# Optimization experiments

Measured on AMD Instinct MI355X. Metric: run time of the kernel, lower is better.

The kernel has to match this reference:

```python
import jax, jax.numpy as jnp
import numpy as np

D_MODEL = 1024
H = 16
D_K = D_MODEL // H
B, S = 1, 4096


def setup_inputs() -> dict:
    key = jax.random.key(0)
    ks = jax.random.split(key, 12)
    std = 1.0 / np.sqrt(D_MODEL)
    inp = {
        "q": jax.random.normal(ks[0], (B, S, D_MODEL), dtype=jnp.float32),
        "k": jax.random.normal(ks[1], (B, S, D_MODEL), dtype=jnp.float32),
        "v": jax.random.normal(ks[2], (B, S, D_MODEL), dtype=jnp.float32),
        "mask": jax.random.randint(ks[3], (B, 1, S, S), 0, 2).astype(bool),
        # nn.Linear params (torch convention: y = x @ W.T + b), weights [out, in]
        "wq": jax.random.uniform(ks[4], (D_MODEL, D_MODEL), jnp.float32, -std, std),
        "bq": jax.random.uniform(ks[5], (D_MODEL,), jnp.float32, -std, std),
        "wk": jax.random.uniform(ks[6], (D_MODEL, D_MODEL), jnp.float32, -std, std),
        "bk": jax.random.uniform(ks[7], (D_MODEL,), jnp.float32, -std, std),
        "wv": jax.random.uniform(ks[8], (D_MODEL, D_MODEL), jnp.float32, -std, std),
        "bv": jax.random.uniform(ks[9], (D_MODEL,), jnp.float32, -std, std),
        "wo": jax.random.uniform(ks[10], (D_MODEL, D_MODEL), jnp.float32, -std, std),
        "bo": jax.random.uniform(ks[11], (D_MODEL,), jnp.float32, -std, std),
    }
    return inp


def _split_heads(x):
    # [b, s, (h d)] -> [b, h, s, d]
    b, s, _ = x.shape
    return x.reshape(b, s, H, D_K).transpose(0, 2, 1, 3)


def reference(q, k, v, mask, wq, bq, wk, bk, wv, bv, wo, bo):
    b, s, d = q.shape
    qh = _split_heads(q @ wq.T + bq)
    kh = _split_heads(k @ wk.T + bk)
    vh = _split_heads(v @ wv.T + bv)
    # NOTE: original scales by sqrt(d_model), not sqrt(d_k) — keep faithful.
    score = jnp.einsum("bhqd,bhkd->bhqk", qh, kh) / jnp.sqrt(jnp.float32(d))
    score = jnp.where(mask, jnp.float32(-1e9), score)
    attn = jax.nn.softmax(score, axis=-1)  # dropout is identity in eval mode
    wv_out = jnp.einsum("bhqk,bhkd->bhqd", attn, vh)
    concat = wv_out.transpose(0, 2, 1, 3).reshape(b, s, d)
    return concat @ wo.T + bo
```

## Files before the change

kernel.cpp:

```cpp
#include <hip/hip_runtime.h>
#include <hip/hip_bf16.h>
#include <math.h>

typedef __attribute__((ext_vector_type(4))) float f32x4;
typedef __attribute__((ext_vector_type(8))) short s16x8;
typedef __attribute__((ext_vector_type(4))) short s16x4;

#define S_LEN 4096
#define DMODEL 1024
#define NHEADS 16
#define DHEAD 64

__device__ __forceinline__ unsigned short f2bf(float f) {
  union { float f; unsigned int u; } x; x.f = f;
  return (unsigned short)((x.u + 0x7FFFu + ((x.u >> 16) & 1u)) >> 16);
}

__device__ __forceinline__ float fexp2(float x) {
#if __has_builtin(__builtin_amdgcn_exp2f)
  return __builtin_amdgcn_exp2f(x);
#else
  float r; asm("v_exp_f32 %0, %1" : "=v"(r) : "v"(x)); return r;
#endif
}

__device__ __forceinline__ void gload_lds16(const void* g, void* l) {
  __builtin_amdgcn_global_load_lds(
      (const __attribute__((address_space(1))) unsigned int*)g,
      (__attribute__((address_space(3))) unsigned int*)l, 16, 0, 0);
}

__global__ __launch_bounds__(256) void mask_pack(const int* __restrict__ mask,
                                                 unsigned long long* __restrict__ bits) {
  const int qr = blockIdx.x;
  const int wv = threadIdx.x >> 6, l = threadIdx.x & 63;
  const int* row = mask + (size_t)qr * S_LEN;
#pragma unroll
  for (int w0 = 0; w0 < 64; w0 += 4) {
    const int w = w0 + wv;
    unsigned long long b = __ballot(row[w * 64 + l] != 0);
    if (l == 0) bits[(size_t)qr * 64 + w] = b;
  }
}

__global__ __launch_bounds__(256) void mask_xpose(const unsigned long long* __restrict__ bits,
                                                  unsigned long long* __restrict__ lmask) {
  const int wv = blockIdx.x * 4 + (threadIdx.x >> 6);
  const int l = threadIdx.x & 63, lr = l & 15, lg4 = (l >> 4) * 4;
  const int qg = wv >> 6, t = wv & 63;
  const unsigned long long rw = bits[(size_t)(qg * 16 + lr) * 64 + t];
  unsigned long long mine = 0;
#pragma unroll
  for (int w = 0; w < 16; ++w) {
    const int sh = (w >> 2) * 16 + (w & 3) + lg4;
    unsigned long long b = __ballot(((rw >> sh) & 1ull) != 0);
    if (l == w) mine = b;
  }
  if (l < 16) lmask[((size_t)qg * 64 + t) * 16 + l] = mine;
}

__global__ __launch_bounds__(256) void cast_bf16(
    const float* __restrict__ s0, const float* __restrict__ s1, const float* __restrict__ s2,
    const float* __restrict__ s3, const float* __restrict__ s4, const float* __restrict__ s5,
    const float* __restrict__ s6, unsigned short* __restrict__ dst) {
  const int z = blockIdx.y;
  const float* src = (z == 0) ? s0 : (z == 1) ? s1 : (z == 2) ? s2 :
                     (z == 3) ? s3 : (z == 4) ? s4 : (z == 5) ? s5 : s6;
  const int n = (z < 3) ? (S_LEN * DMODEL) : (DMODEL * DMODEL);
  unsigned short* d = dst + ((z < 3) ? (size_t)z * S_LEN * DMODEL
                                     : (size_t)3 * S_LEN * DMODEL + (size_t)(z - 3) * DMODEL * DMODEL);
  const int i = (blockIdx.x * 256 + threadIdx.x) * 4;
  if (i < n) {
    f32x4 v = *(const f32x4*)(src + i);
    s16x4 o;
#pragma unroll
    for (int j = 0; j < 4; ++j) o[j] = (short)f2bf(v[j]);
    *(s16x4*)(d + i) = o;
  }
}

template<int A_BF16, int B_BF16, int OUT_MODE>
__device__ __forceinline__ void gemm_body(const void* __restrict__ Ap,
                                          const void* __restrict__ Wp,
                                          const float* __restrict__ bias,
                                          void* __restrict__ outp, float scale) {
  constexpr int K = DMODEL, N = DMODEL, M = S_LEN;
  constexpr int BM = 128, BK = 32, LDT = 40;
  __shared__ unsigned short Alds[BM * LDT];
  __shared__ unsigned short Blds[BM * LDT];
  const int tid = threadIdx.x;
  const int l = tid & 63, wid = tid >> 6;
  const int lr = l & 15, lg = l >> 4;
  const int bm = blockIdx.x * BM;
  const int bn = blockIdx.y * BM;
  const int wm = (wid >> 1) * 64, wn = (wid & 1) * 64;

  f32x4 acc[4][4] = {};

  for (int k0 = 0; k0 < K; k0 += BK) {
    __syncthreads();
    if constexpr (A_BF16) {
      const unsigned short* A = (const unsigned short*)Ap;
      const int col = (tid & 3) * 8, row = tid >> 2;
#pragma unroll
      for (int p = 0; p < 2; ++p) {
        const int r = row + p * 64;
        *(s16x8*)&Alds[r * LDT + col] =
            *(const s16x8*)(A + (size_t)(bm + r) * K + k0 + col);
      }
    } else {
      const float* A = (const float*)Ap;
      const int col = (tid & 7) * 4, row = tid >> 3;
#pragma unroll
      for (int p = 0; p < 4; ++p) {
        const int r = row + p * 32;
        f32x4 vv = *(const f32x4*)(A + (size_t)(bm + r) * K + k0 + col);
        s16x4 o;
#pragma unroll
        for (int j = 0; j < 4; ++j) o[j] = (short)f2bf(vv[j]);
        *(s16x4*)&Alds[r * LDT + col] = o;
      }
    }
    if constexpr (B_BF16) {
      const unsigned short* W = (const unsigned short*)Wp;
      const int col = (tid & 3) * 8, row = tid >> 2;
#pragma unroll
      for (int p = 0; p < 2; ++p) {
        const int r = row + p * 64;
        *(s16x8*)&Blds[r * LDT + col] =
            *(const s16x8*)(W + (size_t)(bn + r) * K + k0 + col);
      }
    } else {
      const float* W = (const float*)Wp;
      const int col = (tid & 7) * 4, row = tid >> 3;
#pragma unroll
      for (int p = 0; p < 4; ++p) {
        const int r = row + p * 32;
        f32x4 vv = *(const f32x4*)(W + (size_t)(bn + r) * K + k0 + col);
        s16x4 o;
#pragma unroll
        for (int j = 0; j < 4; ++j) o[j] = (short)f2bf(vv[j]);
        *(s16x4*)&Blds[r * LDT + col] = o;
      }
    }
    __syncthreads();
    s16x8 af[4], bfr[4];
#pragma unroll
    for (int mi = 0; mi < 4; ++mi)
      af[mi] = *(const s16x8*)&Alds[(wm + mi * 16 + lr) * LDT + lg * 8];
#pragma unroll
    for (int ni = 0; ni < 4; ++ni)
      bfr[ni] = *(const s16x8*)&Blds[(wn + ni * 16 + lr) * LDT + lg * 8];
#pragma unroll
    for (int mi = 0; mi < 4; ++mi)
#pragma unroll
      for (int ni = 0; ni < 4; ++ni)
        acc[mi][ni] = __builtin_amdgcn_mfma_f32_16x16x32_bf16(af[mi], bfr[ni], acc[mi][ni], 0, 0, 0);
  }

#pragma unroll
  for (int ni = 0; ni < 4; ++ni) {
    const int n = bn + wn + ni * 16 + lr;
    const float bv = bias[n];
#pragma unroll
    for (int mi = 0; mi < 4; ++mi) {
#pragma unroll
      for (int j = 0; j < 4; ++j) {
        const int m = bm + wm + mi * 16 + lg * 4 + j;
        const float val = (acc[mi][ni][j] + bv) * scale;
        if constexpr (OUT_MODE == 1) {
          unsigned short* out = (unsigned short*)outp;
          out[((size_t)(n >> 6) * M + m) * DHEAD + (n & 63)] = f2bf(val);
        } else if constexpr (OUT_MODE == 2) {
          unsigned short* out = (unsigned short*)outp;
          out[((size_t)(n >> 6) * DHEAD + (n & 63)) * M + m] = f2bf(val);
        } else {
          float* out = (float*)outp;
          out[(size_t)m * N + n] = val;
        }
      }
    }
  }
}

#define QSCALE 0.04508422f

__global__ __launch_bounds__(256) void proj_qkv_b16(
    const unsigned short* __restrict__ qb, const unsigned short* __restrict__ kb,
    const unsigned short* __restrict__ vb,
    const unsigned short* __restrict__ wqb, const float* __restrict__ bq,
    const unsigned short* __restrict__ wkb, const float* __restrict__ bk,
    const unsigned short* __restrict__ wvb, const float* __restrict__ bv,
    unsigned short* __restrict__ ws) {
  const int z = blockIdx.z;
  if (z == 0)      gemm_body<1, 1, 1>(qb, wqb, bq, ws, QSCALE);
  else if (z == 1) gemm_body<1, 1, 1>(kb, wkb, bk, ws + (size_t)S_LEN * DMODEL, 1.0f);
  else             gemm_body<1, 1, 2>(vb, wvb, bv, ws + (size_t)2 * S_LEN * DMODEL, 1.0f);
}
__global__ __launch_bounds__(256) void outproj_b16(
    const unsigned short* __restrict__ concat, const unsigned short* __restrict__ wob,
    const float* __restrict__ bo, float* __restrict__ out) {
  gemm_body<1, 1, 0>(concat, wob, bo, out, 1.0f);
}
__global__ __launch_bounds__(256) void proj_qkv_f32(
    const float* __restrict__ q, const float* __restrict__ k, const float* __restrict__ v,
    const float* __restrict__ wq, const float* __restrict__ bq,
    const float* __restrict__ wk, const float* __restrict__ bk,
    const float* __restrict__ wv, const float* __restrict__ bv,
    unsigned short* __restrict__ ws) {
  const int z = blockIdx.z;
  if (z == 0)      gemm_body<0, 0, 1>(q, wq, bq, ws, QSCALE);
  else if (z == 1) gemm_body<0, 0, 1>(k, wk, bk, ws + (size_t)S_LEN * DMODEL, 1.0f);
  else             gemm_body<0, 0, 2>(v, wv, bv, ws + (size_t)2 * S_LEN * DMODEL, 1.0f);
}
__global__ __launch_bounds__(256) void outproj_f32(
    const unsigned short* __restrict__ concat, const float* __restrict__ wo,
    const float* __restrict__ bo, float* __restrict__ out) {
  gemm_body<1, 0, 0>(concat, wo, bo, out, 1.0f);
}

template<int NSPLIT>
__global__ __launch_bounds__(512, 4) void attn_fwd(
    const unsigned short* __restrict__ Qh, const unsigned short* __restrict__ Kh,
    const unsigned short* __restrict__ Vt, const unsigned long long* __restrict__ lmask,
    unsigned short* __restrict__ outp,
    float* __restrict__ lpart) {
  __shared__ unsigned short Klds[2][64 * 64];
  __shared__ unsigned short Vlds[2][64 * 64];
  __shared__ unsigned short P_lds[8][32][76];

  const int tid = threadIdx.x;
  const int l = tid & 63, wid = tid >> 6;
  const int lr = l & 15, lg = l >> 4;
  const int per = 32 * NSPLIT;
  const int swz = (blockIdx.x & 7) * per + (blockIdx.x >> 3);
  const int h = swz / (16 * NSPLIT);
  const int split = (NSPLIT == 2) ? ((swz >> 4) & 1) : 0;
  const int qb = swz & 15;
  const int qrow0 = qb * 256 + wid * 32;
  const int kv0 = split * (S_LEN / NSPLIT);
  constexpr int NT = (S_LEN / NSPLIT) / 64;
  const int T0 = kv0 >> 6;

  const unsigned short* Qbase = Qh + ((size_t)h * S_LEN + qrow0) * DHEAD;
  s16x8 qf[2][2];
#pragma unroll
  for (int sub = 0; sub < 2; ++sub)
#pragma unroll
    for (int ds = 0; ds < 2; ++ds)
      qf[sub][ds] = *(const s16x8*)(Qbase + (sub * 16 + lr) * DHEAD + ds * 32 + lg * 8);

  const int wid_u = __builtin_amdgcn_readfirstlane(wid);
  const int qg0 = qb * 16 + wid_u * 2;
  const unsigned long long* mq0 = lmask + (size_t)qg0 * 64 * 16;
  const unsigned long long* mq1 = mq0 + (size_t)64 * 16;

  const int srow = l >> 3;
  const int schunk = (l & 7) ^ srow;
  const unsigned short* Kst = Kh + (size_t)h * S_LEN * DHEAD
                              + (size_t)(kv0 + wid * 8 + srow) * DHEAD + schunk * 8;
  const unsigned short* Vst = Vt + (size_t)h * DHEAD * S_LEN
                              + (size_t)(wid * 8 + srow) * S_LEN + kv0 + schunk * 8;
  const int sdst = (wid * 8) * 64;

  f32x4 o_acc[2][4] = {};
  float lsum[2] = {0.f, 0.f};

  gload_lds16(Kst, &Klds[0][sdst]);
  gload_lds16(Vst, &Vlds[0][sdst]);
  __syncthreads();

  const int xr = lr & 7;

  for (int t = 0; t < NT; ++t) {
    const int buf = t & 1;
    if (t < NT - 1) {
      gload_lds16(Kst + (size_t)(t + 1) * 64 * DHEAD, &Klds[buf ^ 1][sdst]);
      gload_lds16(Vst + (t + 1) * 64, &Vlds[buf ^ 1][sdst]);
    }

    const unsigned short* Kb = &Klds[buf][0];
    f32x4 sc[2][4];
    __builtin_amdgcn_s_setprio(1);
#pragma unroll
    for (int kg = 0; kg < 4; ++kg) {
      const int r = kg * 16 + lr;
      s16x8 k0 = *(const s16x8*)(Kb + r * 64 + ((lg ^ xr) * 8));
      s16x8 k1 = *(const s16x8*)(Kb + r * 64 + (((lg + 4) ^ xr) * 8));
#pragma unroll
      for (int sub = 0; sub < 2; ++sub) {
        f32x4 z = {};
        z = __builtin_amdgcn_mfma_f32_16x16x32_bf16(k0, qf[sub][0], z, 0, 0, 0);
        sc[sub][kg] = __builtin_amdgcn_mfma_f32_16x16x32_bf16(k1, qf[sub][1], z, 0, 0, 0);
      }
    }
    __builtin_amdgcn_s_setprio(0);

    const size_t mo = (size_t)(T0 + t) * 16;
#pragma unroll
    for (int sub = 0; sub < 2; ++sub) {
      const unsigned long long* qp = (sub ? mq1 : mq0) + mo;
#pragma unroll
      for (int kg = 0; kg < 4; ++kg) {
        float p[4];
#pragma unroll
        for (int j = 0; j < 4; ++j) {
          const unsigned long long mw = qp[kg * 4 + j];
          float pv = fexp2(sc[sub][kg][j]);
          asm("v_cndmask_b32 %0, %1, 0, %2" : "=v"(pv) : "v"(pv), "s"(mw));
          p[j] = pv;
          lsum[sub] += pv;
        }
        unsigned int w0, w1;
        asm("v_cvt_pk_bf16_f32 %0, %1, %2" : "=v"(w0) : "v"(p[0]), "v"(p[1]));
        asm("v_cvt_pk_bf16_f32 %0, %1, %2" : "=v"(w1) : "v"(p[2]), "v"(p[3]));
        uint2 pk; pk.x = w0; pk.y = w1;
        *(uint2*)&P_lds[wid][sub * 16 + lr][kg * 16 + lg * 4] = pk;
      }
    }
    asm volatile("s_waitcnt lgkmcnt(0)" ::: "memory");
    __builtin_amdgcn_sched_barrier(0);

    s16x8 pf[2][2];
#pragma unroll
    for (int sub = 0; sub < 2; ++sub)
#pragma unroll
      for (int ks = 0; ks < 2; ++ks)
        pf[sub][ks] = *(const s16x8*)&P_lds[wid][sub * 16 + lr][ks * 32 + lg * 8];

    const unsigned short* Vb = &Vlds[buf][0];
    __builtin_amdgcn_s_setprio(1);
#pragma unroll
    for (int dg = 0; dg < 4; ++dg) {
      const int r = dg * 16 + lr;
      s16x8 v0 = *(const s16x8*)(Vb + r * 64 + ((lg ^ xr) * 8));
      s16x8 v1 = *(const s16x8*)(Vb + r * 64 + (((lg + 4) ^ xr) * 8));
#pragma unroll
      for (int sub = 0; sub < 2; ++sub) {
        o_acc[sub][dg] = __builtin_amdgcn_mfma_f32_16x16x32_bf16(pf[sub][0], v0, o_acc[sub][dg], 0, 0, 0);
        o_acc[sub][dg] = __builtin_amdgcn_mfma_f32_16x16x32_bf16(pf[sub][1], v1, o_acc[sub][dg], 0, 0, 0);
      }
    }
    __builtin_amdgcn_s_setprio(0);

    __syncthreads();
  }

#pragma unroll
  for (int sub = 0; sub < 2; ++sub) {
    lsum[sub] += __shfl_xor(lsum[sub], 16, 64);
    lsum[sub] += __shfl_xor(lsum[sub], 32, 64);
  }

  if constexpr (NSPLIT == 2) {
    unsigned short* op = outp + ((size_t)(split * NHEADS + h) * S_LEN) * DHEAD;
#pragma unroll
    for (int sub = 0; sub < 2; ++sub)
#pragma unroll
      for (int dg = 0; dg < 4; ++dg)
#pragma unroll
        for (int j = 0; j < 4; ++j) {
          const int q = qrow0 + sub * 16 + lg * 4 + j;
          op[(size_t)q * DHEAD + dg * 16 + lr] = f2bf(o_acc[sub][dg][j]);
        }
    if (l < 16) {
      float* lp = lpart + (size_t)(split * NHEADS + h) * S_LEN + qrow0;
      lp[lr] = lsum[0];
      lp[16 + lr] = lsum[1];
    }
  } else {
    float rs[2][4];
#pragma unroll
    for (int sub = 0; sub < 2; ++sub)
#pragma unroll
      for (int j = 0; j < 4; ++j)
        rs[sub][j] = __shfl(lsum[sub], lg * 4 + j, 64);
#pragma unroll
    for (int sub = 0; sub < 2; ++sub)
#pragma unroll
      for (int dg = 0; dg < 4; ++dg)
#pragma unroll
        for (int j = 0; j < 4; ++j) {
          const int q = qrow0 + sub * 16 + lg * 4 + j;
          outp[(size_t)q * DMODEL + h * DHEAD + dg * 16 + lr] =
              f2bf(o_acc[sub][dg][j] / rs[sub][j]);
        }
  }
}

__global__ __launch_bounds__(256) void attn_combine(
    const unsigned short* __restrict__ opart, const float* __restrict__ lpart,
    unsigned short* __restrict__ concat) {
  const int idx = blockIdx.x * 256 + threadIdx.x;
  const int d4 = (idx & 15) * 4;
  const int hq = idx >> 4;
  const int h = hq >> 12, q = hq & 4095;
  const size_t o0 = ((size_t)h * S_LEN + q) * DHEAD + d4;
  const size_t o1 = o0 + (size_t)NHEADS * S_LEN * DHEAD;
  const float linv = 1.0f / (lpart[(size_t)h * S_LEN + q] +
                             lpart[(size_t)(NHEADS + h) * S_LEN + q]);
  s16x4 a = *(const s16x4*)(opart + o0);
  s16x4 b = *(const s16x4*)(opart + o1);
  s16x4 r;
#pragma unroll
  for (int i = 0; i < 4; ++i) {
    union { unsigned int u; float f; } xa, xb;
    xa.u = ((unsigned int)(unsigned short)a[i]) << 16;
    xb.u = ((unsigned int)(unsigned short)b[i]) << 16;
    r[i] = (short)f2bf((xa.f + xb.f) * linv);
  }
  *(s16x4*)(concat + ((size_t)q * DMODEL + h * DHEAD + d4)) = r;
}

extern "C" void kernel_launch(void* const* d_in, const int* in_sizes, int n_in,
                              void* d_out, int out_size, void* d_ws, size_t ws_size,
                              hipStream_t stream) {
  const float* q  = (const float*)d_in[0];
  const float* k  = (const float*)d_in[1];
  const float* v  = (const float*)d_in[2];
  const int* mask = (const int*)d_in[3];
  const float* wq = (const float*)d_in[4];
  const float* bq = (const float*)d_in[5];
  const float* wk = (const float*)d_in[6];
  const float* bk = (const float*)d_in[7];
  const float* wv = (const float*)d_in[8];
  const float* bv = (const float*)d_in[9];
  const float* wo = (const float*)d_in[10];
  const float* bo = (const float*)d_in[11];
  float* out = (float*)d_out;

  const size_t SD = (size_t)S_LEN * DMODEL, DD = (size_t)DMODEL * DMODEL;
  unsigned short* wsq = (unsigned short*)d_ws;
  unsigned short* wsc = wsq + 3 * SD;
  unsigned long long* wslm = (unsigned long long*)(wsc + SD);
  unsigned long long* wsbits = wslm + (size_t)256 * 64 * 16;
  unsigned short* cast0 = (unsigned short*)(wsbits + (size_t)S_LEN * 64);
  const size_t need = (size_t)((char*)(cast0 + 3 * SD + 4 * DD) - (char*)d_ws);
  const bool big = ws_size >= need;

  mask_pack<<<dim3(S_LEN), dim3(256), 0, stream>>>(mask, wsbits);
  mask_xpose<<<dim3(4096), dim3(256), 0, stream>>>(wsbits, wslm);

  if (big) {
    unsigned short* qb  = cast0;
    unsigned short* kb  = qb + SD;
    unsigned short* vb  = kb + SD;
    unsigned short* wqb = vb + SD;
    unsigned short* wkb = wqb + DD;
    unsigned short* wvb = wkb + DD;
    unsigned short* wob = wvb + DD;
    unsigned short* opart = cast0;
    float* lpart = (float*)vb;
    cast_bf16<<<dim3(4096, 7), dim3(256), 0, stream>>>(q, k, v, wq, wk, wv, wo, cast0);
    proj_qkv_b16<<<dim3(32, 8, 3), dim3(256), 0, stream>>>(qb, kb, vb, wqb, bq, wkb, bk, wvb, bv, wsq);
    attn_fwd<2><<<dim3(512), dim3(512), 0, stream>>>(wsq, wsq + SD, wsq + 2 * SD, wslm, opart, lpart);
    attn_combine<<<dim3(4096), dim3(256), 0, stream>>>(opart, lpart, wsc);
    outproj_b16<<<dim3(32, 8), dim3(256), 0, stream>>>(wsc, wob, bo, out);
  } else {
    proj_qkv_f32<<<dim3(32, 8, 3), dim3(256), 0, stream>>>(q, k, v, wq, bq, wk, bk, wv, bv, wsq);
    attn_fwd<1><<<dim3(256), dim3(512), 0, stream>>>(wsq, wsq + SD, wsq + 2 * SD, wslm, wsc, nullptr);
    outproj_f32<<<dim3(32, 8), dim3(256), 0, stream>>>(wsc, wo, bo, out);
  }
}
```

Baseline: 197.6 us.

## Fuse split-attention combine into output projection GEMM A-tile load

Removes the separate attn_combine kernel and the generic outproj GEMM, replacing them with a dedicated output-projection kernel. Its A-operand loader reads the two partial attention outputs and their softmax denominators, normalizes and sums them on the fly, then writes bf16 tiles to LDS. This saves a kernel launch plus a write and re-read of the concat buffer. In exchange, each N-block repeats the combine work and the lpart loads and divides, and the new GEMM is a simple non-pipelined loop that does not use gemm_body's loading path.

```diff
diff --git a/kernel.cpp b/kernel.cpp
--- a/kernel.cpp
+++ b/kernel.cpp
@@ -14,6 +14,11 @@
 __device__ __forceinline__ unsigned short f2bf(float f) {
   union { float f; unsigned int u; } x; x.f = f;
   return (unsigned short)((x.u + 0x7FFFu + ((x.u >> 16) & 1u)) >> 16);
+}
+
+__device__ __forceinline__ float bf2f(unsigned short s) {
+  union { unsigned int u; float f; } x; x.u = ((unsigned int)s) << 16;
+  return x.f;
 }
 
 __device__ __forceinline__ float fexp2(float x) {
@@ -197,11 +202,6 @@
   else if (z == 1) gemm_body<1, 1, 1>(kb, wkb, bk, ws + (size_t)S_LEN * DMODEL, 1.0f);
   else             gemm_body<1, 1, 2>(vb, wvb, bv, ws + (size_t)2 * S_LEN * DMODEL, 1.0f);
 }
-__global__ __launch_bounds__(256) void outproj_b16(
-    const unsigned short* __restrict__ concat, const unsigned short* __restrict__ wob,
-    const float* __restrict__ bo, float* __restrict__ out) {
-  gemm_body<1, 1, 0>(concat, wob, bo, out, 1.0f);
-}
 __global__ __launch_bounds__(256) void proj_qkv_f32(
     const float* __restrict__ q, const float* __restrict__ k, const float* __restrict__ v,
     const float* __restrict__ wq, const float* __restrict__ bq,
@@ -217,6 +217,84 @@
     const unsigned short* __restrict__ concat, const float* __restrict__ wo,
     const float* __restrict__ bo, float* __restrict__ out) {
   gemm_body<1, 0, 0>(concat, wo, bo, out, 1.0f);
+}
+
+__global__ __launch_bounds__(256) void outproj_fused(
+    const unsigned short* __restrict__ opart, const float* __restrict__ lpart,
+    const unsigned short* __restrict__ wob, const float* __restrict__ bo,
+    float* __restrict__ out) {
+  constexpr int K = DMODEL, N = DMODEL;
+  constexpr int BM = 128, BK = 32, LDT = 40;
+  __shared__ unsigned short Alds[BM * LDT];
+  __shared__ unsigned short Blds[BM * LDT];
+  const int tid = threadIdx.x;
+  const int l = tid & 63, wid = tid >> 6;
+  const int lr = l & 15, lg = l >> 4;
+  const int bm = blockIdx.x * BM;
+  const int bn = blockIdx.y * BM;
+  const int wm = (wid >> 1) * 64, wn = (wid & 1) * 64;
+
+  f32x4 acc[4][4] = {};
+  const int colA = (tid & 3) * 8, rowA = tid >> 2;
+  const unsigned short* opart1 = opart + (size_t)NHEADS * S_LEN * DHEAD;
+  const float* lpart1 = lpart + (size_t)NHEADS * S_LEN;
+
+  for (int k0 = 0; k0 < K; k0 += BK) {
+    __syncthreads();
+    {
+      const int k = k0 + colA;
+      const int h = k >> 6, d = k & 63;
+#pragma unroll
+      for (int p = 0; p < 2; ++p) {
+        const int q = bm + rowA + p * 64;
+        const float linv = 1.0f / (lpart[(size_t)h * S_LEN + q] +
+                                   lpart1[(size_t)h * S_LEN + q]);
+        s16x8 a0 = *(const s16x8*)(opart  + ((size_t)h * S_LEN + q) * DHEAD + d);
+        s16x8 a1 = *(const s16x8*)(opart1 + ((size_t)h * S_LEN + q) * DHEAD + d);
+        s16x8 o;
+#pragma unroll
+        for (int j = 0; j < 8; ++j)
+          o[j] = (short)f2bf((bf2f((unsigned short)a0[j]) +
+                              bf2f((unsigned short)a1[j])) * linv);
+        *(s16x8*)&Alds[(rowA + p * 64) * LDT + colA] = o;
+      }
+    }
+    {
+#pragma unroll
+      for (int p = 0; p < 2; ++p) {
+        const int r = rowA + p * 64;
+        *(s16x8*)&Blds[r * LDT + colA] =
+            *(const s16x8*)(wob + (size_t)(bn + r) * K + k0 + colA);
+      }
+    }
+    __syncthreads();
+    s16x8 af[4], bfr[4];
+#pragma unroll
+    for (int mi = 0; mi < 4; ++mi)
+      af[mi] = *(const s16x8*)&Alds[(wm + mi * 16 + lr) * LDT + lg * 8];
+#pragma unroll
+    for (int ni = 0; ni < 4; ++ni)
+      bfr[ni] = *(const s16x8*)&Blds[(wn + ni * 16 + lr) * LDT + lg * 8];
+#pragma unroll
+    for (int mi = 0; mi < 4; ++mi)
+#pragma unroll
+      for (int ni = 0; ni < 4; ++ni)
+        acc[mi][ni] = __builtin_amdgcn_mfma_f32_16x16x32_bf16(af[mi], bfr[ni], acc[mi][ni], 0, 0, 0);
+  }
+
+#pragma unroll
+  for (int ni = 0; ni < 4; ++ni) {
+    const int n = bn + wn + ni * 16 + lr;
+    const float bv = bo[n];
+#pragma unroll
+    for (int mi = 0; mi < 4; ++mi) {
+#pragma unroll
+      for (int j = 0; j < 4; ++j) {
+        const int m = bm + wm + mi * 16 + lg * 4 + j;
+        out[(size_t)m * N + n] = acc[mi][ni][j] + bv;
+      }
+    }
+  }
 }
 
 template<int NSPLIT>
@@ -386,30 +464,6 @@
               f2bf(o_acc[sub][dg][j] / rs[sub][j]);
         }
   }
-}
-
-__global__ __launch_bounds__(256) void attn_combine(
-    const unsigned short* __restrict__ opart, const float* __restrict__ lpart,
-    unsigned short* __restrict__ concat) {
-  const int idx = blockIdx.x * 256 + threadIdx.x;
-  const int d4 = (idx & 15) * 4;
-  const int hq = idx >> 4;
-  const int h = hq >> 12, q = hq & 4095;
-  const size_t o0 = ((size_t)h * S_LEN + q) * DHEAD + d4;
-  const size_t o1 = o0 + (size_t)NHEADS * S_LEN * DHEAD;
-  const float linv = 1.0f / (lpart[(size_t)h * S_LEN + q] +
-                             lpart[(size_t)(NHEADS + h) * S_LEN + q]);
-  s16x4 a = *(const s16x4*)(opart + o0);
-  s16x4 b = *(const s16x4*)(opart + o1);
-  s16x4 r;
-#pragma unroll
-  for (int i = 0; i < 4; ++i) {
-    union { unsigned int u; float f; } xa, xb;
-    xa.u = ((unsigned int)(unsigned short)a[i]) << 16;
-    xb.u = ((unsigned int)(unsigned short)b[i]) << 16;
-    r[i] = (short)f2bf((xa.f + xb.f) * linv);
-  }
-  *(s16x4*)(concat + ((size_t)q * DMODEL + h * DHEAD + d4)) = r;
 }
 
 extern "C" void kernel_launch(void* const* d_in, const int* in_sizes, int n_in,
@@ -454,8 +508,7 @@
     cast_bf16<<<dim3(4096, 7), dim3(256), 0, stream>>>(q, k, v, wq, wk, wv, wo, cast0);
     proj_qkv_b16<<<dim3(32, 8, 3), dim3(256), 0, stream>>>(qb, kb, vb, wqb, bq, wkb, bk, wvb, bv, wsq);
     attn_fwd<2><<<dim3(512), dim3(512), 0, stream>>>(wsq, wsq + SD, wsq + 2 * SD, wslm, opart, lpart);
-    attn_combine<<<dim3(4096), dim3(256), 0, stream>>>(opart, lpart, wsc);
-    outproj_b16<<<dim3(32, 8), dim3(256), 0, stream>>>(wsc, wob, bo, out);
+    outproj_fused<<<dim3(32, 8), dim3(256), 0, stream>>>(opart, lpart, wob, bo, out);
   } else {
     proj_qkv_f32<<<dim3(32, 8, 3), dim3(256), 0, stream>>>(q, k, v, wq, bq, wk, bk, wv, bv, wsq);
     attn_fwd<1><<<dim3(256), dim3(512), 0, stream>>>(wsq, wsq + SD, wsq + 2 * SD, wslm, wsc, nullptr);
```

New measurement: 206.9 us. 1.05x slower.
